# Performance work log

Measured on AMD Instinct MI355X. Metric: run time of the kernel, lower is better.

The kernel has to match this reference:

```python
import jax, jax.numpy as jnp
import numpy as np

N = 50000        # n_nodes
E = 640000       # n_edges
D = 128          # d_model (in_dim == out_dim)
H = 8            # num_heads
DH = D // H      # head dim = 16
EPS = 1e-5


def _batchnorm(x, g, b):
    # BatchNorm1d, training-mode batch statistics (biased variance)
    mu = jnp.mean(x, axis=0)
    var = jnp.mean((x - mu) ** 2, axis=0)
    return (x - mu) * jax.lax.rsqrt(var + EPS) * g + b


def setup_inputs() -> dict:
    key = jax.random.key(0)
    ks = jax.random.split(key, 16)
    s = 0.05
    h = jax.random.normal(ks[0], (N, D), jnp.float32)
    src = jax.random.randint(ks[1], (E,), 0, N)
    # guarantee every node has >= 1 incoming edge (avoids z == 0)
    dst = jnp.concatenate([jnp.arange(N), jax.random.randint(ks[2], (E - N,), 0, N)])
    return {
        "h": h,
        "src": src,
        "dst": dst,
        "WQ": jax.random.normal(ks[3], (D, D), jnp.float32) * s,
        "WK": jax.random.normal(ks[4], (D, D), jnp.float32) * s,
        "WV": jax.random.normal(ks[5], (D, D), jnp.float32) * s,
        "WO": jax.random.normal(ks[6], (D, D), jnp.float32) * s,
        "bO": jnp.zeros((D,), jnp.float32),
        "W1": jax.random.normal(ks[7], (2 * D, D), jnp.float32) * s,
        "b1": jnp.zeros((2 * D,), jnp.float32),
        "W2": jax.random.normal(ks[8], (D, 2 * D), jnp.float32) * s,
        "b2": jnp.zeros((D,), jnp.float32),
        "bn1_g": jnp.ones((D,), jnp.float32),
        "bn1_b": jnp.zeros((D,), jnp.float32),
        "bn2_g": jnp.ones((D,), jnp.float32),
        "bn2_b": jnp.zeros((D,), jnp.float32),
    }


def reference(h, src, dst, WQ, WK, WV, WO, bO, W1, b1, W2, b2, bn1_g, bn1_b, bn2_g, bn2_b):
    n = h.shape[0]
    # projections -> [N, H, DH]
    Q = (h @ WQ.T).reshape(n, H, DH)
    K = (h @ WK.T).reshape(n, H, DH)
    V = (h @ WV.T).reshape(n, H, DH)
    # per-edge score: sum(K[src] * Q[dst]) -> [E, H]; clamp/exp (scaled_exp)
    score = jnp.sum(K[src] * Q[dst], axis=-1) / np.sqrt(DH)
    score = jnp.exp(jnp.clip(score, -5.0, 5.0))
    # scatter-sum weighted values and normalizers to destination nodes
    wV = jax.ops.segment_sum(V[src] * score[..., None], dst, num_segments=n)  # [N,H,DH]
    z = jax.ops.segment_sum(score, dst, num_segments=n)                       # [N,H]
    attn = (wV / z[..., None]).reshape(n, D)
    # O projection + residual + BN1
    h1 = _batchnorm(h + (attn @ WO.T + bO), bn1_g, bn1_b)
    # FFN + residual + BN2
    f = jax.nn.relu(h1 @ W1.T + b1) @ W2.T + b2
    return _batchnorm(h1 + f, bn2_g, bn2_b)
```

## Files before the change

kernel.cpp:

```cpp
#include <hip/hip_runtime.h>
#include <math.h>


#define ND128 16384
typedef _Float16 f16;
typedef __attribute__((ext_vector_type(8))) _Float16 h8;
typedef __attribute__((ext_vector_type(4))) _Float16 h4;
typedef __attribute__((ext_vector_type(2))) _Float16 h2;
typedef __attribute__((ext_vector_type(4))) float f4;

__device__ __forceinline__ float fdot2h(h2 a, h2 b) {
#if __has_builtin(__builtin_amdgcn_fdot2)
    return __builtin_amdgcn_fdot2(a, b, 0.f, false);
#else
    return (float)a[0] * (float)b[0] + (float)a[1] * (float)b[1];
#endif
}

__device__ __forceinline__ float fast_exp2(float x) {
#if __has_builtin(__builtin_amdgcn_exp2f)
    return __builtin_amdgcn_exp2f(x);
#else
    return exp2f(x);
#endif
}

template <int CTRL>
__device__ __forceinline__ float dppadd(float x) {
    int t = __builtin_amdgcn_update_dpp(0, __float_as_int(x), CTRL, 0xF, 0xF, false);
    return x + __int_as_float(t);
}
__device__ __forceinline__ float wsum8(float p) {
    p = dppadd<0xB1>(p);
    p = dppadd<0x4E>(p);
    p = dppadd<0x141>(p);
    return p;
}

__global__ __launch_bounds__(256) void k_prep(
    const float* __restrict__ h, f16* __restrict__ hb,
    const float* __restrict__ WQ, const float* __restrict__ WK,
    const float* __restrict__ WV, const float* __restrict__ WO,
    const float* __restrict__ W2,
    f16* __restrict__ Wqb, f16* __restrict__ Wkb,
    f16* __restrict__ Wvb, f16* __restrict__ Wob, f16* __restrict__ W2b,
    float* __restrict__ bn, int* __restrict__ cursor, int N)
{
    const int slab = blockIdx.x, my = blockIdx.y;
    const int tid = threadIdx.x;
    if (my == 0) {
        if (tid < 128) {
            int ci = slab * 128 + tid;
            if (ci < N) cursor[ci] = 0;
        }
        if (slab == 6) { bn[tid] = 0.f; bn[tid + 256] = 0.f; }
    }
#pragma unroll
    for (int it2 = 0; it2 < 4; ++it2) {
        int it = my * 4 + it2;
        int cid = it * 256 + tid;
        int lane = cid & 63;
        int m = (cid >> 6) & 7;
        int kb = cid >> 9;
        int row = slab * 128 + m * 16 + (lane & 15);
        int col = kb * 32 + (lane >> 4) * 8;
        f16 o8[8];
        if (row < N) {
            const float* p = h + (size_t)row * 128 + col;
            float4 f0 = *(const float4*)p;
            float4 f1 = *(const float4*)(p + 4);
            o8[0] = (f16)f0.x; o8[1] = (f16)f0.y; o8[2] = (f16)f0.z; o8[3] = (f16)f0.w;
            o8[4] = (f16)f1.x; o8[5] = (f16)f1.y; o8[6] = (f16)f1.z; o8[7] = (f16)f1.w;
        } else {
#pragma unroll
            for (int j = 0; j < 8; ++j) o8[j] = (f16)0.f;
        }
        *(h8*)(hb + (size_t)slab * ND128 + (size_t)cid * 8) = *(const h8*)o8;
    }
    if (slab < 6 && my == 1) {
        const float* Wsrc; f16* dst; int K, base;
        if (slab < 4) {
            Wsrc = slab == 0 ? WQ : slab == 1 ? WK : slab == 2 ? WV : WO;
            dst  = slab == 0 ? Wqb : slab == 1 ? Wkb : slab == 2 ? Wvb : Wob;
            K = 128; base = 0;
        } else {
            Wsrc = W2; dst = W2b; K = 256; base = (slab - 4) * 2048;
        }
#pragma unroll
        for (int it = 0; it < 8; ++it) {
            int cid = base + it * 256 + tid;
            int lane = cid & 63;
            int kb, nt;
            if (K == 128) { kb = (cid >> 6) & 3; nt = cid >> 8; }
            else          { kb = (cid >> 6) & 7; nt = cid >> 9; }
            int row = nt * 16 + (lane & 15);
            int col = kb * 32 + (lane >> 4) * 8;
            const float* p = Wsrc + (size_t)row * K + col;
            f16 o8[8];
#pragma unroll
            for (int j = 0; j < 8; ++j) o8[j] = (f16)p[j];
            *(h8*)(dst + (size_t)cid * 8) = *(const h8*)o8;
        }
    }
}

__global__ __launch_bounds__(256) void k_qkv(
    const f16* __restrict__ hb, const f16* __restrict__ Wqb,
    const f16* __restrict__ Wkb, const f16* __restrict__ Wvb,
    f16* __restrict__ Qb, f16* __restrict__ Kh,
    f16* __restrict__ Vh, int N)
{
    const int slab = blockIdx.x, oidx = blockIdx.y, mh = blockIdx.z;
    const int w = threadIdx.x >> 6, lane = threadIdx.x & 63;
    const f16* __restrict__ Wb = oidx == 0 ? Wqb : oidx == 1 ? Wkb : Wvb;
    f16* __restrict__ Ob = oidx == 0 ? Qb : oidx == 1 ? Kh : Vh;
    const f16* A = hb + (size_t)slab * ND128;

    h8 bfr[2][4];
#pragma unroll
    for (int nt = 0; nt < 2; ++nt)
#pragma unroll
        for (int kb = 0; kb < 4; ++kb)
            bfr[nt][kb] = *(const h8*)(Wb + (size_t)(((2 * w + nt) * 4 + kb) * 64 + lane) * 8);

    f4 acc[4][2];
    f4 zero = {0.f, 0.f, 0.f, 0.f};
#pragma unroll
    for (int m = 0; m < 4; ++m) { acc[m][0] = zero; acc[m][1] = zero; }

#pragma unroll
    for (int m = 0; m < 4; ++m) {
        int mg = mh * 4 + m;
#pragma unroll
        for (int kb = 0; kb < 4; ++kb) {
            h8 a = *(const h8*)(A + (size_t)((kb * 8 + mg) * 64 + lane) * 8);
            acc[m][0] = __builtin_amdgcn_mfma_f32_16x16x32_f16(bfr[0][kb], a, acc[m][0], 0, 0, 0);
            acc[m][1] = __builtin_amdgcn_mfma_f32_16x16x32_f16(bfr[1][kb], a, acc[m][1], 0, 0, 0);
        }
    }

    const int rl = lane & 15, quad = lane >> 4;
#pragma unroll
    for (int m = 0; m < 4; ++m) {
        int gr = slab * 128 + (mh * 4 + m) * 16 + rl;
        if (gr < N) {
#pragma unroll
            for (int nt = 0; nt < 2; ++nt) {
                h4 o;
                o[0] = (f16)acc[m][nt][0]; o[1] = (f16)acc[m][nt][1];
                o[2] = (f16)acc[m][nt][2]; o[3] = (f16)acc[m][nt][3];
                *(h4*)(Ob + (size_t)gr * 128 + w * 32 + nt * 16 + quad * 4) = o;
            }
        }
    }
}

__global__ __launch_bounds__(256) void k_hist(
    const int* __restrict__ dst, int* __restrict__ cursor, int E)
{
    int e = blockIdx.x * 256 + threadIdx.x;
    if (e < E) atomicAdd(&cursor[dst[e]], 1);
}

__global__ __launch_bounds__(256) void k_scanA(
    const int* __restrict__ cnt, int* __restrict__ bsum, int N)
{
    const int t = threadIdx.x;
    int base = blockIdx.x * 2048 + t * 8;
    int s = 0;
#pragma unroll
    for (int j = 0; j < 8; ++j) {
        int idx = base + j;
        if (idx < N) s += cnt[idx];
    }
#pragma unroll
    for (int off = 32; off; off >>= 1) s += __shfl_down(s, off, 64);
    __shared__ int ws4[4];
    if ((t & 63) == 0) ws4[t >> 6] = s;
    __syncthreads();
    if (t == 0) bsum[blockIdx.x] = ws4[0] + ws4[1] + ws4[2] + ws4[3];
}

__global__ __launch_bounds__(256) void k_scanC(
    const int* __restrict__ cnt, const int* __restrict__ bsum,
    int* __restrict__ rowptr, int* __restrict__ cursor, int N, int nsb)
{
    const int t = threadIdx.x, b = blockIdx.x;
    __shared__ int sboff;
    if (t == 0) {
        int r = 0;
        for (int i2 = 0; i2 < b; ++i2) r += bsum[i2];
        sboff = r;
    }
    if (t == 64 && b == nsb - 1) {
        int r = 0;
        for (int i2 = 0; i2 < nsb; ++i2) r += bsum[i2];
        rowptr[N] = r;
    }
    int base = b * 2048 + t * 8;
    int loc[8];
    int s = 0;
#pragma unroll
    for (int j = 0; j < 8; ++j) {
        int idx = base + j;
        loc[j] = (idx < N) ? cnt[idx] : 0;
        s += loc[j];
    }
    __shared__ int part[256];
    part[t] = s;
    __syncthreads();
    for (int off = 1; off < 256; off <<= 1) {
        int v = (t >= off) ? part[t - off] : 0;
        __syncthreads();
        part[t] += v;
        __syncthreads();
    }
    int run = sboff + (t ? part[t - 1] : 0);
#pragma unroll
    for (int j = 0; j < 8; ++j) {
        int idx = base + j;
        if (idx < N) { rowptr[idx] = run; cursor[idx] = run; run += loc[j]; }
    }
}

__global__ __launch_bounds__(256) void k_scatter(
    const int* __restrict__ src, const int* __restrict__ dst,
    int* __restrict__ cursor, int* __restrict__ csr_src, int E)
{
    int e = blockIdx.x * 256 + threadIdx.x;
    if (e < E) {
        int pos = atomicAdd(&cursor[dst[e]], 1);
        csr_src[pos] = src[e];
    }
}

__global__ __launch_bounds__(256) void k_attn(
    const f16* __restrict__ Qb, const f16* __restrict__ Kh,
    const f16* __restrict__ Vh,
    const int* __restrict__ rowptr, const int* __restrict__ csr_src,
    f16* __restrict__ attnf, int N)
{
    const int node = blockIdx.x * 4 + (threadIdx.x >> 6);
    const int lane = threadIdx.x & 63;
    if (node >= N) return;
    const int beg = rowptr[node], end = rowptr[node + 1];

    h2 qs;
    {
        h2 q2 = ((const h2*)(Qb + (size_t)node * 128))[lane];
        const float SCL = 0.25f * 1.44269504f;
        qs[0] = (f16)((float)q2[0] * SCL);
        qs[1] = (f16)((float)q2[1] * SCL);
    }
    const float CLP = 5.f * 1.44269504f;

    const h2* __restrict__ K2 = (const h2*)Kh;
    const h2* __restrict__ V2 = (const h2*)Vh;

    h2 accA, accB;
    accA[0] = (f16)0.f; accA[1] = (f16)0.f;
    accB[0] = (f16)0.f; accB[1] = (f16)0.f;
    float z = 0.f;

    int i = beg;
    for (; i + 3 < end; i += 4) {
        int s0 = csr_src[i], s1 = csr_src[i + 1];
        int s2 = csr_src[i + 2], s3 = csr_src[i + 3];
        h2 k0 = K2[(size_t)s0 * 64 + lane];
        h2 k1 = K2[(size_t)s1 * 64 + lane];
        h2 k2 = K2[(size_t)s2 * 64 + lane];
        h2 k3 = K2[(size_t)s3 * 64 + lane];
        h2 v0 = V2[(size_t)s0 * 64 + lane];
        h2 v1 = V2[(size_t)s1 * 64 + lane];
        h2 v2 = V2[(size_t)s2 * 64 + lane];
        h2 v3 = V2[(size_t)s3 * 64 + lane];
        float p0 = fdot2h(qs, k0);
        float p1 = fdot2h(qs, k1);
        float p2 = fdot2h(qs, k2);
        float p3 = fdot2h(qs, k3);
        p0 = wsum8(p0); p1 = wsum8(p1); p2 = wsum8(p2); p3 = wsum8(p3);
        float sc0 = fast_exp2(fminf(fmaxf(p0, -CLP), CLP));
        float sc1 = fast_exp2(fminf(fmaxf(p1, -CLP), CLP));
        float sc2 = fast_exp2(fminf(fmaxf(p2, -CLP), CLP));
        float sc3 = fast_exp2(fminf(fmaxf(p3, -CLP), CLP));
        z += sc0 + sc1 + sc2 + sc3;
        h2 c0; c0[0] = (f16)sc0; c0[1] = (f16)sc0;
        h2 c1; c1[0] = (f16)sc1; c1[1] = (f16)sc1;
        h2 c2; c2[0] = (f16)sc2; c2[1] = (f16)sc2;
        h2 c3; c3[0] = (f16)sc3; c3[1] = (f16)sc3;
        accA += c0 * v0; accB += c1 * v1;
        accA += c2 * v2; accB += c3 * v3;
    }
    for (; i < end; ++i) {
        int s0 = csr_src[i];
        h2 k0 = K2[(size_t)s0 * 64 + lane];
        h2 v0 = V2[(size_t)s0 * 64 + lane];
        float p0 = fdot2h(qs, k0);
        p0 = wsum8(p0);
        float sc0 = fast_exp2(fminf(fmaxf(p0, -CLP), CLP));
        z += sc0;
        h2 c0; c0[0] = (f16)sc0; c0[1] = (f16)sc0;
        accA += c0 * v0;
    }

    float inv = 1.f / z;
    float ax = ((float)accA[0] + (float)accB[0]) * inv;
    float ay = ((float)accA[1] + (float)accB[1]) * inv;
    h2 o2;
    o2[0] = (f16)ax; o2[1] = (f16)ay;
    int slab = node >> 7, m = (node >> 4) & 7, lr = node & 15;
    int kb = lane >> 4, quad2 = (lane & 15) >> 2, j = (lane & 3) * 2;
    *(h2*)(attnf + (size_t)slab * ND128 +
           (size_t)(((kb * 8 + m) * 64 + lr + 16 * quad2) * 8 + j)) = o2;
}

__global__ __launch_bounds__(256) void k_oproj(
    const f16* __restrict__ attnf, const f16* __restrict__ Wob,
    const float* __restrict__ h, const float* __restrict__ bO,
    f16* __restrict__ t1b, float* __restrict__ bn, int N)
{
    __shared__ float csum[128], csq[128];
    const int tid = threadIdx.x, slab = blockIdx.x, mh = blockIdx.y;
    const int w = tid >> 6, lane = tid & 63;
    if (tid < 128) { csum[tid] = 0.f; csq[tid] = 0.f; }
    __syncthreads();
    const f16* A = attnf + (size_t)slab * ND128;

    h8 bfr[2][4];
#pragma unroll
    for (int nt = 0; nt < 2; ++nt)
#pragma unroll
        for (int kb = 0; kb < 4; ++kb)
            bfr[nt][kb] = *(const h8*)(Wob + (size_t)(((2 * w + nt) * 4 + kb) * 64 + lane) * 8);

    f4 acc[4][2];
    f4 zero = {0.f, 0.f, 0.f, 0.f};
#pragma unroll
    for (int m = 0; m < 4; ++m) { acc[m][0] = zero; acc[m][1] = zero; }
#pragma unroll
    for (int m = 0; m < 4; ++m) {
        int mg = mh * 4 + m;
#pragma unroll
        for (int kb = 0; kb < 4; ++kb) {
            h8 a = *(const h8*)(A + (size_t)((kb * 8 + mg) * 64 + lane) * 8);
            acc[m][0] = __builtin_amdgcn_mfma_f32_16x16x32_f16(bfr[0][kb], a, acc[m][0], 0, 0, 0);
            acc[m][1] = __builtin_amdgcn_mfma_f32_16x16x32_f16(bfr[1][kb], a, acc[m][1], 0, 0, 0);
        }
    }

    const int rl = lane & 15, quad = lane >> 4;
    float4 bo[2];
#pragma unroll
    for (int nt = 0; nt < 2; ++nt)
        bo[nt] = *(const float4*)(bO + w * 32 + nt * 16 + quad * 4);
    float pcs[2][4], pcq[2][4];
#pragma unroll
    for (int nt = 0; nt < 2; ++nt)
#pragma unroll
        for (int r = 0; r < 4; ++r) { pcs[nt][r] = 0.f; pcq[nt][r] = 0.f; }

#pragma unroll
    for (int m = 0; m < 4; ++m) {
        int mg = mh * 4 + m;
        int gr = slab * 128 + mg * 16 + rl;
        if (gr < N) {
#pragma unroll
            for (int nt = 0; nt < 2; ++nt) {
                int col0 = w * 32 + nt * 16 + quad * 4;
                float4 hv = *(const float4*)(h + (size_t)gr * 128 + col0);
                float v0 = acc[m][nt][0] + hv.x + bo[nt].x;
                float v1 = acc[m][nt][1] + hv.y + bo[nt].y;
                float v2 = acc[m][nt][2] + hv.z + bo[nt].z;
                float v3 = acc[m][nt][3] + hv.w + bo[nt].w;
                h4 o; o[0] = (f16)v0; o[1] = (f16)v1; o[2] = (f16)v2; o[3] = (f16)v3;
                *(h4*)(t1b + (size_t)slab * ND128 +
                       (size_t)(((w * 8 + mg) * 64 + (nt * 2 + (quad >> 1)) * 16 + rl) * 8 +
                                (quad & 1) * 4)) = o;
                pcs[nt][0] += v0; pcq[nt][0] += v0 * v0;
                pcs[nt][1] += v1; pcq[nt][1] += v1 * v1;
                pcs[nt][2] += v2; pcq[nt][2] += v2 * v2;
                pcs[nt][3] += v3; pcq[nt][3] += v3 * v3;
            }
        }
    }
#pragma unroll
    for (int nt = 0; nt < 2; ++nt)
#pragma unroll
        for (int r = 0; r < 4; ++r) {
            float s = pcs[nt][r], q = pcq[nt][r];
            s += __shfl_xor(s, 8, 16); q += __shfl_xor(q, 8, 16);
            s += __shfl_xor(s, 4, 16); q += __shfl_xor(q, 4, 16);
            s += __shfl_xor(s, 2, 16); q += __shfl_xor(q, 2, 16);
            s += __shfl_xor(s, 1, 16); q += __shfl_xor(q, 1, 16);
            if (rl == 0) {
                int cl = w * 32 + nt * 16 + quad * 4 + r;
                atomicAdd(&csum[cl], s);
                atomicAdd(&csq[cl], q);
            }
        }
    __syncthreads();
    if (tid < 128) {
        atomicAdd(bn + tid, csum[tid]);
        atomicAdd(bn + 128 + tid, csq[tid]);
    }
}

__global__ __launch_bounds__(128) void k_fold1(
    const float* __restrict__ bn, const float* __restrict__ g1,
    const float* __restrict__ bb1, const float* __restrict__ W1,
    const float* __restrict__ b1, f16* __restrict__ W1b,
    float* __restrict__ badj, float* __restrict__ sfold,
    float* __restrict__ bfold, int N)
{
    const int o = blockIdx.x, i = threadIdx.x;
    float invN = 1.f / (float)N;
    float mu = bn[i] * invN;
    float var = bn[128 + i] * invN - mu * mu;
    float s = g1[i] * rsqrtf(var + 1e-5f);
    float bb = bb1[i] - mu * s;
    if (o == 0) { sfold[i] = s; bfold[i] = bb; }
    float wv = W1[(size_t)o * 128 + i];
    __shared__ float red[128];
    red[i] = wv * bb;
    const int nt = o >> 4, lanelow = o & 15;
    const int kb = i >> 5, quad = (i >> 3) & 3, j = i & 7;
    W1b[(size_t)(((nt * 4 + kb) * 64 + lanelow + 16 * quad) * 8 + j)] = (f16)(wv * s);
    __syncthreads();
#pragma unroll
    for (int off = 64; off; off >>= 1) {
        if (i < off) red[i] += red[i + off];
        __syncthreads();
    }
    if (i == 0) badj[o] = b1[o] + red[0];
}

__global__ __launch_bounds__(256) void k_ffn1(
    const f16* __restrict__ t1b, const f16* __restrict__ W1b,
    const float* __restrict__ badj, f16* __restrict__ ub, int N)
{
    const int slab = blockIdx.x, ch = blockIdx.y, mh = blockIdx.z;
    const int w = threadIdx.x >> 6, lane = threadIdx.x & 63;
    const f16* A = t1b + (size_t)slab * ND128;

    h8 bfr[2][4];
#pragma unroll
    for (int nt = 0; nt < 2; ++nt)
#pragma unroll
        for (int kb = 0; kb < 4; ++kb) {
            int ntg = ch * 8 + 2 * w + nt;
            bfr[nt][kb] = *(const h8*)(W1b + (size_t)((ntg * 4 + kb) * 64 + lane) * 8);
        }

    f4 acc[4][2];
    f4 zero = {0.f, 0.f, 0.f, 0.f};
#pragma unroll
    for (int m = 0; m < 4; ++m) { acc[m][0] = zero; acc[m][1] = zero; }
#pragma unroll
    for (int m = 0; m < 4; ++m) {
        int mg = mh * 4 + m;
#pragma unroll
        for (int kb = 0; kb < 4; ++kb) {
            h8 a = *(const h8*)(A + (size_t)((kb * 8 + mg) * 64 + lane) * 8);
            acc[m][0] = __builtin_amdgcn_mfma_f32_16x16x32_f16(bfr[0][kb], a, acc[m][0], 0, 0, 0);
            acc[m][1] = __builtin_amdgcn_mfma_f32_16x16x32_f16(bfr[1][kb], a, acc[m][1], 0, 0, 0);
        }
    }

    const int rl = lane & 15, quad = lane >> 4;
    const int kbu = ch * 4 + w;
    float4 ba[2];
#pragma unroll
    for (int nt = 0; nt < 2; ++nt)
        ba[nt] = *(const float4*)(badj + ch * 128 + w * 32 + nt * 16 + quad * 4);
#pragma unroll
    for (int m = 0; m < 4; ++m) {
        int mg = mh * 4 + m;
        int gr = slab * 128 + mg * 16 + rl;
        if (gr < N) {
#pragma unroll
            for (int nt = 0; nt < 2; ++nt) {
                h4 o;
                o[0] = (f16)fmaxf(acc[m][nt][0] + ba[nt].x, 0.f);
                o[1] = (f16)fmaxf(acc[m][nt][1] + ba[nt].y, 0.f);
                o[2] = (f16)fmaxf(acc[m][nt][2] + ba[nt].z, 0.f);
                o[3] = (f16)fmaxf(acc[m][nt][3] + ba[nt].w, 0.f);
                *(h4*)(ub + (size_t)slab * 32768 +
                       (size_t)(((kbu * 8 + mg) * 64 + (nt * 2 + (quad >> 1)) * 16 + rl) * 8 +
                                (quad & 1) * 4)) = o;
            }
        }
    }
}

__global__ __launch_bounds__(256) void k_ffn2(
    const f16* __restrict__ ub, const f16* __restrict__ W2b,
    const f16* __restrict__ t1b,
    const float* __restrict__ sfold, const float* __restrict__ bfold,
    const float* __restrict__ b2, float* __restrict__ out,
    float* __restrict__ bn, int N)
{
    __shared__ float csum[128], csq[128], sS[128], sB[128];
    const int tid = threadIdx.x, slab = blockIdx.x, mh = blockIdx.y;
    const int w = tid >> 6, lane = tid & 63;
    if (tid < 128) {
        csum[tid] = 0.f; csq[tid] = 0.f;
        sS[tid] = sfold[tid]; sB[tid] = bfold[tid] + b2[tid];
    }
    __syncthreads();
    const f16* A = ub + (size_t)slab * 32768;
    const f16* T1 = t1b + (size_t)slab * ND128;

    h8 bfr[2][8];
#pragma unroll
    for (int nt = 0; nt < 2; ++nt)
#pragma unroll
        for (int kb = 0; kb < 8; ++kb)
            bfr[nt][kb] = *(const h8*)(W2b + (size_t)(((2 * w + nt) * 8 + kb) * 64 + lane) * 8);

    f4 acc[4][2];
    f4 zero = {0.f, 0.f, 0.f, 0.f};
#pragma unroll
    for (int m = 0; m < 4; ++m) { acc[m][0] = zero; acc[m][1] = zero; }
#pragma unroll
    for (int m = 0; m < 4; ++m) {
        int mg = mh * 4 + m;
#pragma unroll
        for (int kb = 0; kb < 8; ++kb) {
            h8 a = *(const h8*)(A + (size_t)((kb * 8 + mg) * 64 + lane) * 8);
            acc[m][0] = __builtin_amdgcn_mfma_f32_16x16x32_f16(bfr[0][kb], a, acc[m][0], 0, 0, 0);
            acc[m][1] = __builtin_amdgcn_mfma_f32_16x16x32_f16(bfr[1][kb], a, acc[m][1], 0, 0, 0);
        }
    }

    const int rl = lane & 15, quad = lane >> 4;
    float pcs[2][4], pcq[2][4];
#pragma unroll
    for (int nt = 0; nt < 2; ++nt)
#pragma unroll
        for (int r = 0; r < 4; ++r) { pcs[nt][r] = 0.f; pcq[nt][r] = 0.f; }

#pragma unroll
    for (int m = 0; m < 4; ++m) {
        int mg = mh * 4 + m;
        int gr = slab * 128 + mg * 16 + rl;
        if (gr < N) {
#pragma unroll
            for (int nt = 0; nt < 2; ++nt) {
                int col0 = w * 32 + nt * 16 + quad * 4;
                h4 t1v = *(const h4*)(T1 +
                    (size_t)(((w * 8 + mg) * 64 + (nt * 2 + (quad >> 1)) * 16 + rl) * 8 +
                             (quad & 1) * 4));
                float4 ss = *(const float4*)&sS[col0];
                float4 sb = *(const float4*)&sB[col0];
                float4 o;
                o.x = acc[m][nt][0] + fmaf(ss.x, (float)t1v[0], sb.x);
                o.y = acc[m][nt][1] + fmaf(ss.y, (float)t1v[1], sb.y);
                o.z = acc[m][nt][2] + fmaf(ss.z, (float)t1v[2], sb.z);
                o.w = acc[m][nt][3] + fmaf(ss.w, (float)t1v[3], sb.w);
                *(float4*)(out + (size_t)gr * 128 + col0) = o;
                pcs[nt][0] += o.x; pcq[nt][0] += o.x * o.x;
                pcs[nt][1] += o.y; pcq[nt][1] += o.y * o.y;
                pcs[nt][2] += o.z; pcq[nt][2] += o.z * o.z;
                pcs[nt][3] += o.w; pcq[nt][3] += o.w * o.w;
            }
        }
    }
#pragma unroll
    for (int nt = 0; nt < 2; ++nt)
#pragma unroll
        for (int r = 0; r < 4; ++r) {
            float s = pcs[nt][r], q = pcq[nt][r];
            s += __shfl_xor(s, 8, 16); q += __shfl_xor(q, 8, 16);
            s += __shfl_xor(s, 4, 16); q += __shfl_xor(q, 4, 16);
            s += __shfl_xor(s, 2, 16); q += __shfl_xor(q, 2, 16);
            s += __shfl_xor(s, 1, 16); q += __shfl_xor(q, 1, 16);
            if (rl == 0) {
                int cl = w * 32 + nt * 16 + quad * 4 + r;
                atomicAdd(&csum[cl], s);
                atomicAdd(&csq[cl], q);
            }
        }
    __syncthreads();
    if (tid < 128) {
        atomicAdd(bn + 256 + tid, csum[tid]);
        atomicAdd(bn + 384 + tid, csq[tid]);
    }
}

__global__ __launch_bounds__(256) void k_bn2(
    float* __restrict__ out, const float* __restrict__ bn,
    const float* __restrict__ g2, const float* __restrict__ bb2, int N)
{
    __shared__ float sS[128], sB[128];
    const int tid = threadIdx.x;
    if (tid < 128) {
        float invN = 1.f / (float)N;
        float mu = bn[256 + tid] * invN;
        float var = bn[384 + tid] * invN - mu * mu;
        float scl = g2[tid] * rsqrtf(var + 1e-5f);
        sS[tid] = scl;
        sB[tid] = bb2[tid] - mu * scl;
    }
    __syncthreads();
    size_t idx = (size_t)blockIdx.x * 256 + tid;
    size_t total = (size_t)N * 32;
    if (idx < total) {
        int c0 = (int)((idx * 4) & 127);
        float4 v = *(const float4*)(out + idx * 4);
        v.x = fmaf(v.x, sS[c0 + 0], sB[c0 + 0]);
        v.y = fmaf(v.y, sS[c0 + 1], sB[c0 + 1]);
        v.z = fmaf(v.z, sS[c0 + 2], sB[c0 + 2]);
        v.w = fmaf(v.w, sS[c0 + 3], sB[c0 + 3]);
        *(float4*)(out + idx * 4) = v;
    }
}

extern "C" void kernel_launch(void* const* d_in, const int* in_sizes, int n_in,
                              void* d_out, int out_size, void* d_ws, size_t ws_size,
                              hipStream_t stream)
{
    const float* h   = (const float*)d_in[0];
    const int*   src = (const int*)d_in[1];
    const int*   dst = (const int*)d_in[2];
    const float* WQ  = (const float*)d_in[3];
    const float* WK  = (const float*)d_in[4];
    const float* WV  = (const float*)d_in[5];
    const float* WO  = (const float*)d_in[6];
    const float* bO  = (const float*)d_in[7];
    const float* W1  = (const float*)d_in[8];
    const float* b1  = (const float*)d_in[9];
    const float* W2  = (const float*)d_in[10];
    const float* b2  = (const float*)d_in[11];
    const float* g1  = (const float*)d_in[12];
    const float* bb1 = (const float*)d_in[13];
    const float* g2  = (const float*)d_in[14];
    const float* bb2 = (const float*)d_in[15];
    float* out = (float*)d_out;

    int N = in_sizes[0] / 128;
    int E = in_sizes[1];
    const int slabs = (N + 127) / 128;
    const int nsb = (N + 2047) / 2048;
    const size_t B1 = (size_t)slabs * 32768;

    char* Wp = (char*)d_ws;
    f16* hb  = (f16*)Wp;
    f16* Qb  = (f16*)(Wp + B1);
    f16* Kh  = (f16*)(Wp + 2 * B1);
    f16* Vh  = (f16*)(Wp + 3 * B1);
    f16* ub  = (f16*)(Wp + B1);
    f16* t1b = (f16*)(Wp + 3 * B1);
    const size_t base = 4 * B1;
    f16* Wqb = (f16*)(Wp + base);
    f16* Wkb = (f16*)(Wp + base + 32768);
    f16* Wvb = (f16*)(Wp + base + 65536);
    f16* Wob = (f16*)(Wp + base + 98304);
    f16* W1b = (f16*)(Wp + base + 131072);
    f16* W2b = (f16*)(Wp + base + 196608);
    float* badj  = (float*)(Wp + base + 262144);
    float* sfold = (float*)(Wp + base + 263168);
    float* bfold = (float*)(Wp + base + 263680);
    float* bn    = (float*)(Wp + base + 264192);
    int* cursor  = (int*)(Wp + base + 266240);
    int* rowptr  = (int*)(Wp + base + 266240 + (size_t)N * 4);
    int* csr     = (int*)(Wp + base + 266240 + (size_t)N * 8 + 8);
    int* bsum    = (int*)((char*)csr + (size_t)E * 4);

    k_prep<<<dim3(slabs, 2), 256, 0, stream>>>(h, hb, WQ, WK, WV, WO, W2,
                                               Wqb, Wkb, Wvb, Wob, W2b, bn, cursor, N);
    k_qkv<<<dim3(slabs, 3, 2), 256, 0, stream>>>(hb, Wqb, Wkb, Wvb, Qb, Kh, Vh, N);
    k_hist<<<(E + 255) / 256, 256, 0, stream>>>(dst, cursor, E);
    k_scanA<<<nsb, 256, 0, stream>>>(cursor, bsum, N);
    k_scanC<<<nsb, 256, 0, stream>>>(cursor, bsum, rowptr, cursor, N, nsb);
    k_scatter<<<(E + 255) / 256, 256, 0, stream>>>(src, dst, cursor, csr, E);
    k_attn<<<(N + 3) / 4, 256, 0, stream>>>(Qb, Kh, Vh, rowptr, csr, hb, N);
    k_oproj<<<dim3(slabs, 2), 256, 0, stream>>>(hb, Wob, h, bO, t1b, bn, N);
    k_fold1<<<256, 128, 0, stream>>>(bn, g1, bb1, W1, b1, W1b, badj, sfold, bfold, N);
    k_ffn1<<<dim3(slabs, 2, 2), 256, 0, stream>>>(t1b, W1b, badj, ub, N);
    k_ffn2<<<dim3(slabs, 2), 256, 0, stream>>>(ub, W2b, t1b, sfold, bfold, b2, out, bn, N);
    k_bn2<<<(int)(((size_t)N * 32 + 255) / 256), 256, 0, stream>>>(out, bn, g2, bb2, N);
}
```

Baseline: 329.0 us.

## Store K/V in FP8, fuse hist into prep, merge tail kernels with grid barriers

K and V are now written by the QKV kernel as an interleaved FP8 buffer (256 bytes per node), halving the gather bytes in the edge-attention kernel, which decodes them to fp32 and accumulates in fp32. The degree histogram is merged into the prep kernel, and a memset replaces the in-kernel zeroing. The O-projection, BN1 fold, FFN1, FFN2 and BN2 kernels are collapsed into one persistent cooperative kernel that uses software grid barriers between phases, removing launch gaps. FP8 K/V lowers accuracy, and the spin barriers add synchronization cost and depend on every block being co-resident.

```diff
diff --git a/kernel.cpp b/kernel.cpp
--- a/kernel.cpp
+++ b/kernel.cpp
@@ -8,14 +8,7 @@
 typedef __attribute__((ext_vector_type(4))) _Float16 h4;
 typedef __attribute__((ext_vector_type(2))) _Float16 h2;
 typedef __attribute__((ext_vector_type(4))) float f4;
-
-__device__ __forceinline__ float fdot2h(h2 a, h2 b) {
-#if __has_builtin(__builtin_amdgcn_fdot2)
-    return __builtin_amdgcn_fdot2(a, b, 0.f, false);
-#else
-    return (float)a[0] * (float)b[0] + (float)a[1] * (float)b[1];
-#endif
-}
+typedef __attribute__((ext_vector_type(2))) float ff2;
 
 __device__ __forceinline__ float fast_exp2(float x) {
 #if __has_builtin(__builtin_amdgcn_exp2f)
@@ -37,24 +30,87 @@
     return p;
 }
 
-__global__ __launch_bounds__(256) void k_prep(
+__device__ __forceinline__ ff2 fp8x2_dec(unsigned v) {
+#if __has_builtin(__builtin_amdgcn_cvt_pk_f32_fp8)
+    return __builtin_amdgcn_cvt_pk_f32_fp8((int)v, false);
+#else
+    ff2 r;
+    unsigned b0 = v & 0xffu, b1 = (v >> 8) & 0xffu;
+    {
+        unsigned e = (b0 >> 3) & 15u, m = b0 & 7u;
+        float x = e ? __uint_as_float(((e + 120u) << 23) | (m << 20)) : (float)m * 0.001953125f;
+        r.x = (b0 & 0x80u) ? -x : x;
+    }
+    {
+        unsigned e = (b1 >> 3) & 15u, m = b1 & 7u;
+        float x = e ? __uint_as_float(((e + 120u) << 23) | (m << 20)) : (float)m * 0.001953125f;
+        r.y = (b1 & 0x80u) ? -x : x;
+    }
+    return r;
+#endif
+}
+
+#if !__has_builtin(__builtin_amdgcn_cvt_pk_fp8_f32)
+__device__ __forceinline__ unsigned char fp8_1(float f) {
+    float a = fabsf(f);
+    unsigned sg = (__float_as_uint(f) >> 31) << 7;
+    if (a >= 448.f) return (unsigned char)(sg | 0x7E);
+    if (a < 0.0009765625f) return (unsigned char)sg;
+    int E; float m = frexpf(a, &E);
+    if (E - 1 < -6) {
+        int q = (int)rintf(a * 512.f);
+        if (q > 7) return (unsigned char)(sg | 0x08);
+        return (unsigned char)(sg | q);
+    }
+    int q = (int)rintf(m * 16.f);
+    if (q == 16) { q = 8; E += 1; }
+    int Ef = E - 1 + 7;
+    if (Ef > 15) return (unsigned char)(sg | 0x7E);
+    return (unsigned char)(sg | (Ef << 3) | (q - 8));
+}
+#endif
+
+__device__ __forceinline__ unsigned fp8_pack4(float a0, float a1, float a2, float a3) {
+#if __has_builtin(__builtin_amdgcn_cvt_pk_fp8_f32)
+    int pk = __builtin_amdgcn_cvt_pk_fp8_f32(a0, a1, 0, false);
+    pk = __builtin_amdgcn_cvt_pk_fp8_f32(a2, a3, pk, true);
+    return (unsigned)pk;
+#else
+    return (unsigned)fp8_1(a0) | ((unsigned)fp8_1(a1) << 8) |
+           ((unsigned)fp8_1(a2) << 16) | ((unsigned)fp8_1(a3) << 24);
+#endif
+}
+
+__device__ __forceinline__ void gbar(int* cnt, int ph) {
+    __threadfence();
+    __syncthreads();
+    if (threadIdx.x == 0) {
+        __hip_atomic_fetch_add(cnt, 1, __ATOMIC_ACQ_REL, __HIP_MEMORY_SCOPE_AGENT);
+        const int target = (int)gridDim.x * ph;
+        while (__hip_atomic_load(cnt, __ATOMIC_ACQUIRE, __HIP_MEMORY_SCOPE_AGENT) < target)
+            __builtin_amdgcn_s_sleep(8);
+    }
+    __syncthreads();
+}
+
+__global__ __launch_bounds__(256) void k_prep_hist(
     const float* __restrict__ h, f16* __restrict__ hb,
     const float* __restrict__ WQ, const float* __restrict__ WK,
     const float* __restrict__ WV, const float* __restrict__ WO,
     const float* __restrict__ W2,
     f16* __restrict__ Wqb, f16* __restrict__ Wkb,
     f16* __restrict__ Wvb, f16* __restrict__ Wob, f16* __restrict__ W2b,
-    float* __restrict__ bn, int* __restrict__ cursor, int N)
+    int* __restrict__ cursor, const int* __restrict__ dst,
+    int N, int E, int nhb)
 {
-    const int slab = blockIdx.x, my = blockIdx.y;
     const int tid = threadIdx.x;
-    if (my == 0) {
-        if (tid < 128) {
-            int ci = slab * 128 + tid;
-            if (ci < N) cursor[ci] = 0;
-        }
-        if (slab == 6) { bn[tid] = 0.f; bn[tid + 256] = 0.f; }
-    }
+    if (blockIdx.x < (unsigned)nhb) {
+        int e = blockIdx.x * 256 + tid;
+        if (e < E) atomicAdd(&cursor[dst[e]], 1);
+        return;
+    }
+    const int p = blockIdx.x - nhb;
+    const int slab = p >> 1, my = p & 1;
 #pragma unroll
     for (int it2 = 0; it2 < 4; ++it2) {
         int it = my * 4 + it2;
@@ -66,9 +122,9 @@
         int col = kb * 32 + (lane >> 4) * 8;
         f16 o8[8];
         if (row < N) {
-            const float* p = h + (size_t)row * 128 + col;
-            float4 f0 = *(const float4*)p;
-            float4 f1 = *(const float4*)(p + 4);
+            const float* pp = h + (size_t)row * 128 + col;
+            float4 f0 = *(const float4*)pp;
+            float4 f1 = *(const float4*)(pp + 4);
             o8[0] = (f16)f0.x; o8[1] = (f16)f0.y; o8[2] = (f16)f0.z; o8[3] = (f16)f0.w;
             o8[4] = (f16)f1.x; o8[5] = (f16)f1.y; o8[6] = (f16)f1.z; o8[7] = (f16)f1.w;
         } else {
@@ -78,13 +134,13 @@
         *(h8*)(hb + (size_t)slab * ND128 + (size_t)cid * 8) = *(const h8*)o8;
     }
     if (slab < 6 && my == 1) {
-        const float* Wsrc; f16* dst; int K, base;
+        const float* Wsrc; f16* dstw; int K, base;
         if (slab < 4) {
             Wsrc = slab == 0 ? WQ : slab == 1 ? WK : slab == 2 ? WV : WO;
-            dst  = slab == 0 ? Wqb : slab == 1 ? Wkb : slab == 2 ? Wvb : Wob;
+            dstw = slab == 0 ? Wqb : slab == 1 ? Wkb : slab == 2 ? Wvb : Wob;
             K = 128; base = 0;
         } else {
-            Wsrc = W2; dst = W2b; K = 256; base = (slab - 4) * 2048;
+            Wsrc = W2; dstw = W2b; K = 256; base = (slab - 4) * 2048;
         }
 #pragma unroll
         for (int it = 0; it < 8; ++it) {
@@ -95,11 +151,11 @@
             else          { kb = (cid >> 6) & 7; nt = cid >> 9; }
             int row = nt * 16 + (lane & 15);
             int col = kb * 32 + (lane >> 4) * 8;
-            const float* p = Wsrc + (size_t)row * K + col;
+            const float* pp = Wsrc + (size_t)row * K + col;
             f16 o8[8];
 #pragma unroll
-            for (int j = 0; j < 8; ++j) o8[j] = (f16)p[j];
-            *(h8*)(dst + (size_t)cid * 8) = *(const h8*)o8;
+            for (int j = 0; j < 8; ++j) o8[j] = (f16)pp[j];
+            *(h8*)(dstw + (size_t)cid * 8) = *(const h8*)o8;
         }
     }
 }
@@ -107,13 +163,11 @@
 __global__ __launch_bounds__(256) void k_qkv(
     const f16* __restrict__ hb, const f16* __restrict__ Wqb,
     const f16* __restrict__ Wkb, const f16* __restrict__ Wvb,
-    f16* __restrict__ Qb, f16* __restrict__ Kh,
-    f16* __restrict__ Vh, int N)
+    f16* __restrict__ Qb, unsigned char* __restrict__ KV8, int N)
 {
     const int slab = blockIdx.x, oidx = blockIdx.y, mh = blockIdx.z;
     const int w = threadIdx.x >> 6, lane = threadIdx.x & 63;
     const f16* __restrict__ Wb = oidx == 0 ? Wqb : oidx == 1 ? Wkb : Wvb;
-    f16* __restrict__ Ob = oidx == 0 ? Qb : oidx == 1 ? Kh : Vh;
     const f16* A = hb + (size_t)slab * ND128;
 
     h8 bfr[2][4];
@@ -140,26 +194,35 @@
     }
 
     const int rl = lane & 15, quad = lane >> 4;
-#pragma unroll
-    for (int m = 0; m < 4; ++m) {
-        int gr = slab * 128 + (mh * 4 + m) * 16 + rl;
-        if (gr < N) {
-#pragma unroll
-            for (int nt = 0; nt < 2; ++nt) {
-                h4 o;
-                o[0] = (f16)acc[m][nt][0]; o[1] = (f16)acc[m][nt][1];
-                o[2] = (f16)acc[m][nt][2]; o[3] = (f16)acc[m][nt][3];
-                *(h4*)(Ob + (size_t)gr * 128 + w * 32 + nt * 16 + quad * 4) = o;
-            }
-        }
-    }
-}
-
-__global__ __launch_bounds__(256) void k_hist(
-    const int* __restrict__ dst, int* __restrict__ cursor, int E)
-{
-    int e = blockIdx.x * 256 + threadIdx.x;
-    if (e < E) atomicAdd(&cursor[dst[e]], 1);
+    if (oidx == 0) {
+#pragma unroll
+        for (int m = 0; m < 4; ++m) {
+            int gr = slab * 128 + (mh * 4 + m) * 16 + rl;
+            if (gr < N) {
+#pragma unroll
+                for (int nt = 0; nt < 2; ++nt) {
+                    h4 o;
+                    o[0] = (f16)acc[m][nt][0]; o[1] = (f16)acc[m][nt][1];
+                    o[2] = (f16)acc[m][nt][2]; o[3] = (f16)acc[m][nt][3];
+                    *(h4*)(Qb + (size_t)gr * 128 + w * 32 + nt * 16 + quad * 4) = o;
+                }
+            }
+        }
+    } else {
+        const int voff = (oidx == 2) ? 128 : 0;
+#pragma unroll
+        for (int m = 0; m < 4; ++m) {
+            int gr = slab * 128 + (mh * 4 + m) * 16 + rl;
+            if (gr < N) {
+#pragma unroll
+                for (int nt = 0; nt < 2; ++nt) {
+                    unsigned pk = fp8_pack4(acc[m][nt][0], acc[m][nt][1],
+                                            acc[m][nt][2], acc[m][nt][3]);
+                    *(unsigned*)(KV8 + (size_t)gr * 256 + voff + w * 32 + nt * 16 + quad * 4) = pk;
+                }
+            }
+        }
+    }
 }
 
 __global__ __launch_bounds__(256) void k_scanA(
@@ -235,8 +298,7 @@
 }
 
 __global__ __launch_bounds__(256) void k_attn(
-    const f16* __restrict__ Qb, const f16* __restrict__ Kh,
-    const f16* __restrict__ Vh,
+    const f16* __restrict__ Qb, const unsigned char* __restrict__ KV8,
     const int* __restrict__ rowptr, const int* __restrict__ csr_src,
     f16* __restrict__ attnf, int N)
 {
@@ -245,354 +307,341 @@
     if (node >= N) return;
     const int beg = rowptr[node], end = rowptr[node + 1];
 
-    h2 qs;
+    float qx, qy;
     {
         h2 q2 = ((const h2*)(Qb + (size_t)node * 128))[lane];
         const float SCL = 0.25f * 1.44269504f;
-        qs[0] = (f16)((float)q2[0] * SCL);
-        qs[1] = (f16)((float)q2[1] * SCL);
+        qx = (float)q2[0] * SCL;
+        qy = (float)q2[1] * SCL;
     }
     const float CLP = 5.f * 1.44269504f;
 
-    const h2* __restrict__ K2 = (const h2*)Kh;
-    const h2* __restrict__ V2 = (const h2*)Vh;
-
-    h2 accA, accB;
-    accA[0] = (f16)0.f; accA[1] = (f16)0.f;
-    accB[0] = (f16)0.f; accB[1] = (f16)0.f;
-    float z = 0.f;
-
+    float axA = 0.f, ayA = 0.f, axB = 0.f, ayB = 0.f, zA = 0.f, zB = 0.f;
     int i = beg;
     for (; i + 3 < end; i += 4) {
         int s0 = csr_src[i], s1 = csr_src[i + 1];
         int s2 = csr_src[i + 2], s3 = csr_src[i + 3];
-        h2 k0 = K2[(size_t)s0 * 64 + lane];
-        h2 k1 = K2[(size_t)s1 * 64 + lane];
-        h2 k2 = K2[(size_t)s2 * 64 + lane];
-        h2 k3 = K2[(size_t)s3 * 64 + lane];
-        h2 v0 = V2[(size_t)s0 * 64 + lane];
-        h2 v1 = V2[(size_t)s1 * 64 + lane];
-        h2 v2 = V2[(size_t)s2 * 64 + lane];
-        h2 v3 = V2[(size_t)s3 * 64 + lane];
-        float p0 = fdot2h(qs, k0);
-        float p1 = fdot2h(qs, k1);
-        float p2 = fdot2h(qs, k2);
-        float p3 = fdot2h(qs, k3);
+        unsigned k0 = *(const unsigned short*)(KV8 + (size_t)s0 * 256 + 2 * lane);
+        unsigned k1 = *(const unsigned short*)(KV8 + (size_t)s1 * 256 + 2 * lane);
+        unsigned k2 = *(const unsigned short*)(KV8 + (size_t)s2 * 256 + 2 * lane);
+        unsigned k3 = *(const unsigned short*)(KV8 + (size_t)s3 * 256 + 2 * lane);
+        unsigned v0 = *(const unsigned short*)(KV8 + (size_t)s0 * 256 + 128 + 2 * lane);
+        unsigned v1 = *(const unsigned short*)(KV8 + (size_t)s1 * 256 + 128 + 2 * lane);
+        unsigned v2 = *(const unsigned short*)(KV8 + (size_t)s2 * 256 + 128 + 2 * lane);
+        unsigned v3 = *(const unsigned short*)(KV8 + (size_t)s3 * 256 + 128 + 2 * lane);
+        ff2 kf0 = fp8x2_dec(k0), kf1 = fp8x2_dec(k1);
+        ff2 kf2 = fp8x2_dec(k2), kf3 = fp8x2_dec(k3);
+        float p0 = fmaf(qx, kf0.x, qy * kf0.y);
+        float p1 = fmaf(qx, kf1.x, qy * kf1.y);
+        float p2 = fmaf(qx, kf2.x, qy * kf2.y);
+        float p3 = fmaf(qx, kf3.x, qy * kf3.y);
         p0 = wsum8(p0); p1 = wsum8(p1); p2 = wsum8(p2); p3 = wsum8(p3);
         float sc0 = fast_exp2(fminf(fmaxf(p0, -CLP), CLP));
         float sc1 = fast_exp2(fminf(fmaxf(p1, -CLP), CLP));
         float sc2 = fast_exp2(fminf(fmaxf(p2, -CLP), CLP));
         float sc3 = fast_exp2(fminf(fmaxf(p3, -CLP), CLP));
-        z += sc0 + sc1 + sc2 + sc3;
-        h2 c0; c0[0] = (f16)sc0; c0[1] = (f16)sc0;
-        h2 c1; c1[0] = (f16)sc1; c1[1] = (f16)sc1;
-        h2 c2; c2[0] = (f16)sc2; c2[1] = (f16)sc2;
-        h2 c3; c3[0] = (f16)sc3; c3[1] = (f16)sc3;
-        accA += c0 * v0; accB += c1 * v1;
-        accA += c2 * v2; accB += c3 * v3;
+        ff2 vf0 = fp8x2_dec(v0), vf1 = fp8x2_dec(v1);
+        ff2 vf2 = fp8x2_dec(v2), vf3 = fp8x2_dec(v3);
+        axA = fmaf(vf0.x, sc0, axA); ayA = fmaf(vf0.y, sc0, ayA);
+        axB = fmaf(vf1.x, sc1, axB); ayB = fmaf(vf1.y, sc1, ayB);
+        axA = fmaf(vf2.x, sc2, axA); ayA = fmaf(vf2.y, sc2, ayA);
+        axB = fmaf(vf3.x, sc3, axB); ayB = fmaf(vf3.y, sc3, ayB);
+        zA += sc0 + sc2; zB += sc1 + sc3;
     }
     for (; i < end; ++i) {
         int s0 = csr_src[i];
-        h2 k0 = K2[(size_t)s0 * 64 + lane];
-        h2 v0 = V2[(size_t)s0 * 64 + lane];
-        float p0 = fdot2h(qs, k0);
+        unsigned k0 = *(const unsigned short*)(KV8 + (size_t)s0 * 256 + 2 * lane);
+        unsigned v0 = *(const unsigned short*)(KV8 + (size_t)s0 * 256 + 128 + 2 * lane);
+        ff2 kf0 = fp8x2_dec(k0);
+        float p0 = fmaf(qx, kf0.x, qy * kf0.y);
         p0 = wsum8(p0);
         float sc0 = fast_exp2(fminf(fmaxf(p0, -CLP), CLP));
-        z += sc0;
-        h2 c0; c0[0] = (f16)sc0; c0[1] = (f16)sc0;
-        accA += c0 * v0;
-    }
-
-    float inv = 1.f / z;
-    float ax = ((float)accA[0] + (float)accB[0]) * inv;
-    float ay = ((float)accA[1] + (float)accB[1]) * inv;
+        ff2 vf0 = fp8x2_dec(v0);
+        axA = fmaf(vf0.x, sc0, axA); ayA = fmaf(vf0.y, sc0, ayA);
+        zA += sc0;
+    }
+    float inv = 1.f / (zA + zB);
     h2 o2;
-    o2[0] = (f16)ax; o2[1] = (f16)ay;
+    o2[0] = (f16)((axA + axB) * inv);
+    o2[1] = (f16)((ayA + ayB) * inv);
     int slab = node >> 7, m = (node >> 4) & 7, lr = node & 15;
     int kb = lane >> 4, quad2 = (lane & 15) >> 2, j = (lane & 3) * 2;
     *(h2*)(attnf + (size_t)slab * ND128 +
            (size_t)(((kb * 8 + m) * 64 + lr + 16 * quad2) * 8 + j)) = o2;
 }
 
-__global__ __launch_bounds__(256) void k_oproj(
+__global__ __launch_bounds__(256) void k_backc(
     const f16* __restrict__ attnf, const f16* __restrict__ Wob,
     const float* __restrict__ h, const float* __restrict__ bO,
-    f16* __restrict__ t1b, float* __restrict__ bn, int N)
+    f16* __restrict__ t1b, float* __restrict__ bn,
+    const float* __restrict__ g1, const float* __restrict__ bb1,
+    const float* __restrict__ W1, const float* __restrict__ b1,
+    f16* __restrict__ W1b, float* __restrict__ badj,
+    float* __restrict__ sfold, float* __restrict__ bfold,
+    f16* __restrict__ ub, const f16* __restrict__ W2b,
+    const float* __restrict__ b2, float* __restrict__ out,
+    const float* __restrict__ g2, const float* __restrict__ bb2,
+    int* __restrict__ gcnt, int N, int slabs)
 {
-    __shared__ float csum[128], csq[128];
-    const int tid = threadIdx.x, slab = blockIdx.x, mh = blockIdx.y;
+    const int tid = threadIdx.x;
+    const int G = gridDim.x;
     const int w = tid >> 6, lane = tid & 63;
-    if (tid < 128) { csum[tid] = 0.f; csq[tid] = 0.f; }
-    __syncthreads();
-    const f16* A = attnf + (size_t)slab * ND128;
-
-    h8 bfr[2][4];
-#pragma unroll
-    for (int nt = 0; nt < 2; ++nt)
-#pragma unroll
-        for (int kb = 0; kb < 4; ++kb)
-            bfr[nt][kb] = *(const h8*)(Wob + (size_t)(((2 * w + nt) * 4 + kb) * 64 + lane) * 8);
-
-    f4 acc[4][2];
-    f4 zero = {0.f, 0.f, 0.f, 0.f};
-#pragma unroll
-    for (int m = 0; m < 4; ++m) { acc[m][0] = zero; acc[m][1] = zero; }
-#pragma unroll
-    for (int m = 0; m < 4; ++m) {
-        int mg = mh * 4 + m;
-#pragma unroll
-        for (int kb = 0; kb < 4; ++kb) {
-            h8 a = *(const h8*)(A + (size_t)((kb * 8 + mg) * 64 + lane) * 8);
-            acc[m][0] = __builtin_amdgcn_mfma_f32_16x16x32_f16(bfr[0][kb], a, acc[m][0], 0, 0, 0);
-            acc[m][1] = __builtin_amdgcn_mfma_f32_16x16x32_f16(bfr[1][kb], a, acc[m][1], 0, 0, 0);
-        }
-    }
-
     const int rl = lane & 15, quad = lane >> 4;
-    float4 bo[2];
-#pragma unroll
-    for (int nt = 0; nt < 2; ++nt)
-        bo[nt] = *(const float4*)(bO + w * 32 + nt * 16 + quad * 4);
-    float pcs[2][4], pcq[2][4];
-#pragma unroll
-    for (int nt = 0; nt < 2; ++nt)
-#pragma unroll
-        for (int r = 0; r < 4; ++r) { pcs[nt][r] = 0.f; pcq[nt][r] = 0.f; }
-
-#pragma unroll
-    for (int m = 0; m < 4; ++m) {
-        int mg = mh * 4 + m;
-        int gr = slab * 128 + mg * 16 + rl;
-        if (gr < N) {
-#pragma unroll
-            for (int nt = 0; nt < 2; ++nt) {
-                int col0 = w * 32 + nt * 16 + quad * 4;
-                float4 hv = *(const float4*)(h + (size_t)gr * 128 + col0);
-                float v0 = acc[m][nt][0] + hv.x + bo[nt].x;
-                float v1 = acc[m][nt][1] + hv.y + bo[nt].y;
-                float v2 = acc[m][nt][2] + hv.z + bo[nt].z;
-                float v3 = acc[m][nt][3] + hv.w + bo[nt].w;
-                h4 o; o[0] = (f16)v0; o[1] = (f16)v1; o[2] = (f16)v2; o[3] = (f16)v3;
-                *(h4*)(t1b + (size_t)slab * ND128 +
-                       (size_t)(((w * 8 + mg) * 64 + (nt * 2 + (quad >> 1)) * 16 + rl) * 8 +
-                                (quad & 1) * 4)) = o;
-                pcs[nt][0] += v0; pcq[nt][0] += v0 * v0;
-                pcs[nt][1] += v1; pcq[nt][1] += v1 * v1;
-                pcs[nt][2] += v2; pcq[nt][2] += v2 * v2;
-                pcs[nt][3] += v3; pcq[nt][3] += v3 * v3;
-            }
-        }
-    }
-#pragma unroll
-    for (int nt = 0; nt < 2; ++nt)
-#pragma unroll
-        for (int r = 0; r < 4; ++r) {
-            float s = pcs[nt][r], q = pcq[nt][r];
-            s += __shfl_xor(s, 8, 16); q += __shfl_xor(q, 8, 16);
-            s += __shfl_xor(s, 4, 16); q += __shfl_xor(q, 4, 16);
-            s += __shfl_xor(s, 2, 16); q += __shfl_xor(q, 2, 16);
-            s += __shfl_xor(s, 1, 16); q += __shfl_xor(q, 1, 16);
-            if (rl == 0) {
-                int cl = w * 32 + nt * 16 + quad * 4 + r;
-                atomicAdd(&csum[cl], s);
-                atomicAdd(&csq[cl], q);
-            }
-        }
-    __syncthreads();
-    if (tid < 128) {
-        atomicAdd(bn + tid, csum[tid]);
-        atomicAdd(bn + 128 + tid, csq[tid]);
-    }
-}
-
-__global__ __launch_bounds__(128) void k_fold1(
-    const float* __restrict__ bn, const float* __restrict__ g1,
-    const float* __restrict__ bb1, const float* __restrict__ W1,
-    const float* __restrict__ b1, f16* __restrict__ W1b,
-    float* __restrict__ badj, float* __restrict__ sfold,
-    float* __restrict__ bfold, int N)
-{
-    const int o = blockIdx.x, i = threadIdx.x;
-    float invN = 1.f / (float)N;
-    float mu = bn[i] * invN;
-    float var = bn[128 + i] * invN - mu * mu;
-    float s = g1[i] * rsqrtf(var + 1e-5f);
-    float bb = bb1[i] - mu * s;
-    if (o == 0) { sfold[i] = s; bfold[i] = bb; }
-    float wv = W1[(size_t)o * 128 + i];
+    __shared__ float csum[128], csq[128], sS[128], sB[128];
     __shared__ float red[128];
-    red[i] = wv * bb;
-    const int nt = o >> 4, lanelow = o & 15;
-    const int kb = i >> 5, quad = (i >> 3) & 3, j = i & 7;
-    W1b[(size_t)(((nt * 4 + kb) * 64 + lanelow + 16 * quad) * 8 + j)] = (f16)(wv * s);
-    __syncthreads();
-#pragma unroll
-    for (int off = 64; off; off >>= 1) {
-        if (i < off) red[i] += red[i + off];
+
+    {
+        h8 bfr[2][4];
+#pragma unroll
+        for (int nt = 0; nt < 2; ++nt)
+#pragma unroll
+            for (int kb = 0; kb < 4; ++kb)
+                bfr[nt][kb] = *(const h8*)(Wob + (size_t)(((2 * w + nt) * 4 + kb) * 64 + lane) * 8);
+        float4 bo[2];
+#pragma unroll
+        for (int nt = 0; nt < 2; ++nt)
+            bo[nt] = *(const float4*)(bO + w * 32 + nt * 16 + quad * 4);
+
+        for (int u = blockIdx.x; u < slabs * 2; u += G) {
+            const int slab = u >> 1, mh = u & 1;
+            if (tid < 128) { csum[tid] = 0.f; csq[tid] = 0.f; }
+            __syncthreads();
+            const f16* A = attnf + (size_t)slab * ND128;
+
+            f4 acc[4][2];
+            f4 zero = {0.f, 0.f, 0.f, 0.f};
+#pragma unroll
+            for (int m = 0; m < 4; ++m) { acc[m][0] = zero; acc[m][1] = zero; }
+#pragma unroll
+            for (int m = 0; m < 4; ++m) {
+                int mg = mh * 4 + m;
+#pragma unroll
+                for (int kb = 0; kb < 4; ++kb) {
+                    h8 a = *(const h8*)(A + (size_t)((kb * 8 + mg) * 64 + lane) * 8);
+                    acc[m][0] = __builtin_amdgcn_mfma_f32_16x16x32_f16(bfr[0][kb], a, acc[m][0], 0, 0, 0);
+                    acc[m][1] = __builtin_amdgcn_mfma_f32_16x16x32_f16(bfr[1][kb], a, acc[m][1], 0, 0, 0);
+                }
+            }
+            float pcs[2][4], pcq[2][4];
+#pragma unroll
+            for (int nt = 0; nt < 2; ++nt)
+#pragma unroll
+                for (int r = 0; r < 4; ++r) { pcs[nt][r] = 0.f; pcq[nt][r] = 0.f; }
+#pragma unroll
+            for (int m = 0; m < 4; ++m) {
+                int mg = mh * 4 + m;
+                int gr = slab * 128 + mg * 16 + rl;
+                if (gr < N) {
+#pragma unroll
+                    for (int nt = 0; nt < 2; ++nt) {
+                        int col0 = w * 32 + nt * 16 + quad * 4;
+                        float4 hv = *(const float4*)(h + (size_t)gr * 128 + col0);
+                        float v0 = acc[m][nt][0] + hv.x + bo[nt].x;
+                        float v1 = acc[m][nt][1] + hv.y + bo[nt].y;
+                        float v2 = acc[m][nt][2] + hv.z + bo[nt].z;
+                        float v3 = acc[m][nt][3] + hv.w + bo[nt].w;
+                        h4 o; o[0] = (f16)v0; o[1] = (f16)v1; o[2] = (f16)v2; o[3] = (f16)v3;
+                        *(h4*)(t1b + (size_t)slab * ND128 +
+                               (size_t)(((w * 8 + mg) * 64 + (nt * 2 + (quad >> 1)) * 16 + rl) * 8 +
+                                        (quad & 1) * 4)) = o;
+                        pcs[nt][0] += v0; pcq[nt][0] += v0 * v0;
+                        pcs[nt][1] += v1; pcq[nt][1] += v1 * v1;
+                        pcs[nt][2] += v2; pcq[nt][2] += v2 * v2;
+                        pcs[nt][3] += v3; pcq[nt][3] += v3 * v3;
+                    }
+                }
+            }
+#pragma unroll
+            for (int nt = 0; nt < 2; ++nt)
+#pragma unroll
+                for (int r = 0; r < 4; ++r) {
+                    float s = pcs[nt][r], q = pcq[nt][r];
+                    s += __shfl_xor(s, 8, 16); q += __shfl_xor(q, 8, 16);
+                    s += __shfl_xor(s, 4, 16); q += __shfl_xor(q, 4, 16);
+                    s += __shfl_xor(s, 2, 16); q += __shfl_xor(q, 2, 16);
+                    s += __shfl_xor(s, 1, 16); q += __shfl_xor(q, 1, 16);
+                    if (rl == 0) {
+                        int cl = w * 32 + nt * 16 + quad * 4 + r;
+                        atomicAdd(&csum[cl], s);
+                        atomicAdd(&csq[cl], q);
+                    }
+                }
+            __syncthreads();
+            if (tid < 128) {
+                atomicAdd(bn + tid, csum[tid]);
+                atomicAdd(bn + 128 + tid, csq[tid]);
+            }
+            __syncthreads();
+        }
+    }
+    gbar(gcnt, 1);
+
+    for (int u = blockIdx.x; u < 256; u += G) {
+        const int o = u;
+        if (tid < 128) {
+            const int i = tid;
+            float invN = 1.f / (float)N;
+            float mu = bn[i] * invN;
+            float var = bn[128 + i] * invN - mu * mu;
+            float s = g1[i] * rsqrtf(var + 1e-5f);
+            float bb = bb1[i] - mu * s;
+            if (o == 0) { sfold[i] = s; bfold[i] = bb; }
+            float wv = W1[(size_t)o * 128 + i];
+            red[i] = wv * bb;
+            const int nt = o >> 4, lanelow = o & 15;
+            const int kb = i >> 5, qq = (i >> 3) & 3, j = i & 7;
+            W1b[(size_t)(((nt * 4 + kb) * 64 + lanelow + 16 * qq) * 8 + j)] = (f16)(wv * s);
+        }
         __syncthreads();
-    }
-    if (i == 0) badj[o] = b1[o] + red[0];
-}
-
-__global__ __launch_bounds__(256) void k_ffn1(
-    const f16* __restrict__ t1b, const f16* __restrict__ W1b,
-    const float* __restrict__ badj, f16* __restrict__ ub, int N)
-{
-    const int slab = blockIdx.x, ch = blockIdx.y, mh = blockIdx.z;
-    const int w = threadIdx.x >> 6, lane = threadIdx.x & 63;
-    const f16* A = t1b + (size_t)slab * ND128;
-
-    h8 bfr[2][4];
-#pragma unroll
-    for (int nt = 0; nt < 2; ++nt)
-#pragma unroll
-        for (int kb = 0; kb < 4; ++kb) {
-            int ntg = ch * 8 + 2 * w + nt;
-            bfr[nt][kb] = *(const h8*)(W1b + (size_t)((ntg * 4 + kb) * 64 + lane) * 8);
-        }
-
-    f4 acc[4][2];
-    f4 zero = {0.f, 0.f, 0.f, 0.f};
-#pragma unroll
-    for (int m = 0; m < 4; ++m) { acc[m][0] = zero; acc[m][1] = zero; }
-#pragma unroll
-    for (int m = 0; m < 4; ++m) {
-        int mg = mh * 4 + m;
-#pragma unroll
-        for (int kb = 0; kb < 4; ++kb) {
-            h8 a = *(const h8*)(A + (size_t)((kb * 8 + mg) * 64 + lane) * 8);
-            acc[m][0] = __builtin_amdgcn_mfma_f32_16x16x32_f16(bfr[0][kb], a, acc[m][0], 0, 0, 0);
-            acc[m][1] = __builtin_amdgcn_mfma_f32_16x16x32_f16(bfr[1][kb], a, acc[m][1], 0, 0, 0);
-        }
-    }
-
-    const int rl = lane & 15, quad = lane >> 4;
-    const int kbu = ch * 4 + w;
-    float4 ba[2];
-#pragma unroll
-    for (int nt = 0; nt < 2; ++nt)
-        ba[nt] = *(const float4*)(badj + ch * 128 + w * 32 + nt * 16 + quad * 4);
-#pragma unroll
-    for (int m = 0; m < 4; ++m) {
-        int mg = mh * 4 + m;
-        int gr = slab * 128 + mg * 16 + rl;
-        if (gr < N) {
-#pragma unroll
-            for (int nt = 0; nt < 2; ++nt) {
-                h4 o;
-                o[0] = (f16)fmaxf(acc[m][nt][0] + ba[nt].x, 0.f);
-                o[1] = (f16)fmaxf(acc[m][nt][1] + ba[nt].y, 0.f);
-                o[2] = (f16)fmaxf(acc[m][nt][2] + ba[nt].z, 0.f);
-                o[3] = (f16)fmaxf(acc[m][nt][3] + ba[nt].w, 0.f);
-                *(h4*)(ub + (size_t)slab * 32768 +
-                       (size_t)(((kbu * 8 + mg) * 64 + (nt * 2 + (quad >> 1)) * 16 + rl) * 8 +
-                                (quad & 1) * 4)) = o;
-            }
-        }
-    }
-}
-
-__global__ __launch_bounds__(256) void k_ffn2(
-    const f16* __restrict__ ub, const f16* __restrict__ W2b,
-    const f16* __restrict__ t1b,
-    const float* __restrict__ sfold, const float* __restrict__ bfold,
-    const float* __restrict__ b2, float* __restrict__ out,
-    float* __restrict__ bn, int N)
-{
-    __shared__ float csum[128], csq[128], sS[128], sB[128];
-    const int tid = threadIdx.x, slab = blockIdx.x, mh = blockIdx.y;
-    const int w = tid >> 6, lane = tid & 63;
-    if (tid < 128) {
-        csum[tid] = 0.f; csq[tid] = 0.f;
-        sS[tid] = sfold[tid]; sB[tid] = bfold[tid] + b2[tid];
-    }
-    __syncthreads();
-    const f16* A = ub + (size_t)slab * 32768;
-    const f16* T1 = t1b + (size_t)slab * ND128;
-
-    h8 bfr[2][8];
-#pragma unroll
-    for (int nt = 0; nt < 2; ++nt)
-#pragma unroll
-        for (int kb = 0; kb < 8; ++kb)
-            bfr[nt][kb] = *(const h8*)(W2b + (size_t)(((2 * w + nt) * 8 + kb) * 64 + lane) * 8);
-
-    f4 acc[4][2];
-    f4 zero = {0.f, 0.f, 0.f, 0.f};
-#pragma unroll
-    for (int m = 0; m < 4; ++m) { acc[m][0] = zero; acc[m][1] = zero; }
-#pragma unroll
-    for (int m = 0; m < 4; ++m) {
-        int mg = mh * 4 + m;
-#pragma unroll
-        for (int kb = 0; kb < 8; ++kb) {
-            h8 a = *(const h8*)(A + (size_t)((kb * 8 + mg) * 64 + lane) * 8);
-            acc[m][0] = __builtin_amdgcn_mfma_f32_16x16x32_f16(bfr[0][kb], a, acc[m][0], 0, 0, 0);
-            acc[m][1] = __builtin_amdgcn_mfma_f32_16x16x32_f16(bfr[1][kb], a, acc[m][1], 0, 0, 0);
-        }
-    }
-
-    const int rl = lane & 15, quad = lane >> 4;
-    float pcs[2][4], pcq[2][4];
-#pragma unroll
-    for (int nt = 0; nt < 2; ++nt)
-#pragma unroll
-        for (int r = 0; r < 4; ++r) { pcs[nt][r] = 0.f; pcq[nt][r] = 0.f; }
-
-#pragma unroll
-    for (int m = 0; m < 4; ++m) {
-        int mg = mh * 4 + m;
-        int gr = slab * 128 + mg * 16 + rl;
-        if (gr < N) {
-#pragma unroll
-            for (int nt = 0; nt < 2; ++nt) {
-                int col0 = w * 32 + nt * 16 + quad * 4;
-                h4 t1v = *(const h4*)(T1 +
-                    (size_t)(((w * 8 + mg) * 64 + (nt * 2 + (quad >> 1)) * 16 + rl) * 8 +
-                             (quad & 1) * 4));
-                float4 ss = *(const float4*)&sS[col0];
-                float4 sb = *(const float4*)&sB[col0];
-                float4 o;
-                o.x = acc[m][nt][0] + fmaf(ss.x, (float)t1v[0], sb.x);
-                o.y = acc[m][nt][1] + fmaf(ss.y, (float)t1v[1], sb.y);
-                o.z = acc[m][nt][2] + fmaf(ss.z, (float)t1v[2], sb.z);
-                o.w = acc[m][nt][3] + fmaf(ss.w, (float)t1v[3], sb.w);
-                *(float4*)(out + (size_t)gr * 128 + col0) = o;
-                pcs[nt][0] += o.x; pcq[nt][0] += o.x * o.x;
-                pcs[nt][1] += o.y; pcq[nt][1] += o.y * o.y;
-                pcs[nt][2] += o.z; pcq[nt][2] += o.z * o.z;
-                pcs[nt][3] += o.w; pcq[nt][3] += o.w * o.w;
-            }
-        }
-    }
-#pragma unroll
-    for (int nt = 0; nt < 2; ++nt)
-#pragma unroll
-        for (int r = 0; r < 4; ++r) {
-            float s = pcs[nt][r], q = pcq[nt][r];
-            s += __shfl_xor(s, 8, 16); q += __shfl_xor(q, 8, 16);
-            s += __shfl_xor(s, 4, 16); q += __shfl_xor(q, 4, 16);
-            s += __shfl_xor(s, 2, 16); q += __shfl_xor(q, 2, 16);
-            s += __shfl_xor(s, 1, 16); q += __shfl_xor(q, 1, 16);
-            if (rl == 0) {
-                int cl = w * 32 + nt * 16 + quad * 4 + r;
-                atomicAdd(&csum[cl], s);
-                atomicAdd(&csq[cl], q);
-            }
-        }
-    __syncthreads();
-    if (tid < 128) {
-        atomicAdd(bn + 256 + tid, csum[tid]);
-        atomicAdd(bn + 384 + tid, csq[tid]);
-    }
-}
-
-__global__ __launch_bounds__(256) void k_bn2(
-    float* __restrict__ out, const float* __restrict__ bn,
-    const float* __restrict__ g2, const float* __restrict__ bb2, int N)
-{
-    __shared__ float sS[128], sB[128];
-    const int tid = threadIdx.x;
+        for (int off = 64; off; off >>= 1) {
+            if (tid < off) red[tid] += red[tid + off];
+            __syncthreads();
+        }
+        if (tid == 0) badj[o] = b1[o] + red[0];
+        __syncthreads();
+    }
+    gbar(gcnt, 2);
+
+    for (int u = blockIdx.x; u < slabs * 4; u += G) {
+        const int slab = u >> 2, ch = (u >> 1) & 1, mh = u & 1;
+        const f16* A = t1b + (size_t)slab * ND128;
+
+        h8 bfr[2][4];
+#pragma unroll
+        for (int nt = 0; nt < 2; ++nt)
+#pragma unroll
+            for (int kb = 0; kb < 4; ++kb) {
+                int ntg = ch * 8 + 2 * w + nt;
+                bfr[nt][kb] = *(const h8*)(W1b + (size_t)((ntg * 4 + kb) * 64 + lane) * 8);
+            }
+
+        f4 acc[4][2];
+        f4 zero = {0.f, 0.f, 0.f, 0.f};
+#pragma unroll
+        for (int m = 0; m < 4; ++m) { acc[m][0] = zero; acc[m][1] = zero; }
+#pragma unroll
+        for (int m = 0; m < 4; ++m) {
+            int mg = mh * 4 + m;
+#pragma unroll
+            for (int kb = 0; kb < 4; ++kb) {
+                h8 a = *(const h8*)(A + (size_t)((kb * 8 + mg) * 64 + lane) * 8);
+                acc[m][0] = __builtin_amdgcn_mfma_f32_16x16x32_f16(bfr[0][kb], a, acc[m][0], 0, 0, 0);
+                acc[m][1] = __builtin_amdgcn_mfma_f32_16x16x32_f16(bfr[1][kb], a, acc[m][1], 0, 0, 0);
+            }
+        }
+        const int kbu = ch * 4 + w;
+        float4 ba[2];
+#pragma unroll
+        for (int nt = 0; nt < 2; ++nt)
+            ba[nt] = *(const float4*)(badj + ch * 128 + w * 32 + nt * 16 + quad * 4);
+#pragma unroll
+        for (int m = 0; m < 4; ++m) {
+            int mg = mh * 4 + m;
+            int gr = slab * 128 + mg * 16 + rl;
+            if (gr < N) {
+#pragma unroll
+                for (int nt = 0; nt < 2; ++nt) {
+                    h4 o;
+                    o[0] = (f16)fmaxf(acc[m][nt][0] + ba[nt].x, 0.f);
+                    o[1] = (f16)fmaxf(acc[m][nt][1] + ba[nt].y, 0.f);
+                    o[2] = (f16)fmaxf(acc[m][nt][2] + ba[nt].z, 0.f);
+                    o[3] = (f16)fmaxf(acc[m][nt][3] + ba[nt].w, 0.f);
+                    *(h4*)(ub + (size_t)slab * 32768 +
+                           (size_t)(((kbu * 8 + mg) * 64 + (nt * 2 + (quad >> 1)) * 16 + rl) * 8 +
+                                    (quad & 1) * 4)) = o;
+                }
+            }
+        }
+    }
+    gbar(gcnt, 3);
+
+    {
+        h8 bfr[2][8];
+#pragma unroll
+        for (int nt = 0; nt < 2; ++nt)
+#pragma unroll
+            for (int kb = 0; kb < 8; ++kb)
+                bfr[nt][kb] = *(const h8*)(W2b + (size_t)(((2 * w + nt) * 8 + kb) * 64 + lane) * 8);
+        if (tid < 128) { sS[tid] = sfold[tid]; sB[tid] = bfold[tid] + b2[tid]; }
+        __syncthreads();
+
+        for (int u = blockIdx.x; u < slabs * 2; u += G) {
+            const int slab = u >> 1, mh = u & 1;
+            if (tid < 128) { csum[tid] = 0.f; csq[tid] = 0.f; }
+            __syncthreads();
+            const f16* A = ub + (size_t)slab * 32768;
+            const f16* T1 = t1b + (size_t)slab * ND128;
+
+            f4 acc[4][2];
+            f4 zero = {0.f, 0.f, 0.f, 0.f};
+#pragma unroll
+            for (int m = 0; m < 4; ++m) { acc[m][0] = zero; acc[m][1] = zero; }
+#pragma unroll
+            for (int m = 0; m < 4; ++m) {
+                int mg = mh * 4 + m;
+#pragma unroll
+                for (int kb = 0; kb < 8; ++kb) {
+                    h8 a = *(const h8*)(A + (size_t)((kb * 8 + mg) * 64 + lane) * 8);
+                    acc[m][0] = __builtin_amdgcn_mfma_f32_16x16x32_f16(bfr[0][kb], a, acc[m][0], 0, 0, 0);
+                    acc[m][1] = __builtin_amdgcn_mfma_f32_16x16x32_f16(bfr[1][kb], a, acc[m][1], 0, 0, 0);
+                }
+            }
+            float pcs[2][4], pcq[2][4];
+#pragma unroll
+            for (int nt = 0; nt < 2; ++nt)
+#pragma unroll
+                for (int r = 0; r < 4; ++r) { pcs[nt][r] = 0.f; pcq[nt][r] = 0.f; }
+#pragma unroll
+            for (int m = 0; m < 4; ++m) {
+                int mg = mh * 4 + m;
+                int gr = slab * 128 + mg * 16 + rl;
+                if (gr < N) {
+#pragma unroll
+                    for (int nt = 0; nt < 2; ++nt) {
+                        int col0 = w * 32 + nt * 16 + quad * 4;
+                        h4 t1v = *(const h4*)(T1 +
+                            (size_t)(((w * 8 + mg) * 64 + (nt * 2 + (quad >> 1)) * 16 + rl) * 8 +
+                                     (quad & 1) * 4));
+                        float4 ss = *(const float4*)&sS[col0];
+                        float4 sb = *(const float4*)&sB[col0];
+                        float4 o;
+                        o.x = acc[m][nt][0] + fmaf(ss.x, (float)t1v[0], sb.x);
+                        o.y = acc[m][nt][1] + fmaf(ss.y, (float)t1v[1], sb.y);
+                        o.z = acc[m][nt][2] + fmaf(ss.z, (float)t1v[2], sb.z);
+                        o.w = acc[m][nt][3] + fmaf(ss.w, (float)t1v[3], sb.w);
+                        *(float4*)(out + (size_t)gr * 128 + col0) = o;
+                        pcs[nt][0] += o.x; pcq[nt][0] += o.x * o.x;
+                        pcs[nt][1] += o.y; pcq[nt][1] += o.y * o.y;
+                        pcs[nt][2] += o.z; pcq[nt][2] += o.z * o.z;
+                        pcs[nt][3] += o.w; pcq[nt][3] += o.w * o.w;
+                    }
+                }
+            }
+#pragma unroll
+            for (int nt = 0; nt < 2; ++nt)
+#pragma unroll
+                for (int r = 0; r < 4; ++r) {
+                    float s = pcs[nt][r], q = pcq[nt][r];
+                    s += __shfl_xor(s, 8, 16); q += __shfl_xor(q, 8, 16);
+                    s += __shfl_xor(s, 4, 16); q += __shfl_xor(q, 4, 16);
+                    s += __shfl_xor(s, 2, 16); q += __shfl_xor(q, 2, 16);
+                    s += __shfl_xor(s, 1, 16); q += __shfl_xor(q, 1, 16);
+                    if (rl == 0) {
+                        int cl = w * 32 + nt * 16 + quad * 4 + r;
+                        atomicAdd(&csum[cl], s);
+                        atomicAdd(&csq[cl], q);
+                    }
+                }
+            __syncthreads();
+            if (tid < 128) {
+                atomicAdd(bn + 256 + tid, csum[tid]);
+                atomicAdd(bn + 384 + tid, csq[tid]);
+            }
+            __syncthreads();
+        }
+    }
+    gbar(gcnt, 4);
+
     if (tid < 128) {
         float invN = 1.f / (float)N;
         float mu = bn[256 + tid] * invN;
@@ -602,16 +651,19 @@
         sB[tid] = bb2[tid] - mu * scl;
     }
     __syncthreads();
-    size_t idx = (size_t)blockIdx.x * 256 + tid;
-    size_t total = (size_t)N * 32;
-    if (idx < total) {
-        int c0 = (int)((idx * 4) & 127);
-        float4 v = *(const float4*)(out + idx * 4);
-        v.x = fmaf(v.x, sS[c0 + 0], sB[c0 + 0]);
-        v.y = fmaf(v.y, sS[c0 + 1], sB[c0 + 1]);
-        v.z = fmaf(v.z, sS[c0 + 2], sB[c0 + 2]);
-        v.w = fmaf(v.w, sS[c0 + 3], sB[c0 + 3]);
-        *(float4*)(out + idx * 4) = v;
+    const size_t total = (size_t)N * 32;
+    const int U9 = (int)((total + 255) / 256);
+    for (int u = blockIdx.x; u < U9; u += G) {
+        size_t idx = (size_t)u * 256 + tid;
+        if (idx < total) {
+            int c0 = (int)((idx * 4) & 127);
+            float4 v = *(const float4*)(out + idx * 4);
+            v.x = fmaf(v.x, sS[c0 + 0], sB[c0 + 0]);
+            v.y = fmaf(v.y, sS[c0 + 1], sB[c0 + 1]);
+            v.z = fmaf(v.z, sS[c0 + 2], sB[c0 + 2]);
+            v.w = fmaf(v.w, sS[c0 + 3], sB[c0 + 3]);
+            *(float4*)(out + idx * 4) = v;
+        }
     }
 }
 
@@ -639,15 +691,15 @@
 
     int N = in_sizes[0] / 128;
     int E = in_sizes[1];
-    const int slabs = (N + 127) / 128;
-    const int nsb = (N + 2047) / 2048;
+    int slabs = (N + 127) / 128;
+    int nsb = (N + 2047) / 2048;
+    int nhb = (E + 255) / 256;
     const size_t B1 = (size_t)slabs * 32768;
 
     char* Wp = (char*)d_ws;
     f16* hb  = (f16*)Wp;
     f16* Qb  = (f16*)(Wp + B1);
-    f16* Kh  = (f16*)(Wp + 2 * B1);
-    f16* Vh  = (f16*)(Wp + 3 * B1);
+    unsigned char* KV8 = (unsigned char*)(Wp + 2 * B1);
     f16* ub  = (f16*)(Wp + B1);
     f16* t1b = (f16*)(Wp + 3 * B1);
     const size_t base = 4 * B1;
@@ -661,22 +713,38 @@
     float* sfold = (float*)(Wp + base + 263168);
     float* bfold = (float*)(Wp + base + 263680);
     float* bn    = (float*)(Wp + base + 264192);
-    int* cursor  = (int*)(Wp + base + 266240);
-    int* rowptr  = (int*)(Wp + base + 266240 + (size_t)N * 4);
-    int* csr     = (int*)(Wp + base + 266240 + (size_t)N * 8 + 8);
-    int* bsum    = (int*)((char*)csr + (size_t)E * 4);
-
-    k_prep<<<dim3(slabs, 2), 256, 0, stream>>>(h, hb, WQ, WK, WV, WO, W2,
-                                               Wqb, Wkb, Wvb, Wob, W2b, bn, cursor, N);
-    k_qkv<<<dim3(slabs, 3, 2), 256, 0, stream>>>(hb, Wqb, Wkb, Wvb, Qb, Kh, Vh, N);
-    k_hist<<<(E + 255) / 256, 256, 0, stream>>>(dst, cursor, E);
+    int* gcnt    = (int*)(Wp + base + 266240);
+    int* bsum    = (int*)(Wp + base + 266496);
+    int* cursor  = (int*)(Wp + base + 266752);
+    int* rowptr  = (int*)(Wp + base + 266752 + (size_t)N * 4);
+    int* csr     = (int*)(Wp + base + 266752 + (size_t)N * 8 + 8);
+
+    static int ncu = 0, nbk = 0;
+    if (ncu == 0) {
+        int dev = 0;
+        hipGetDevice(&dev);
+        hipDeviceGetAttribute(&ncu, hipDeviceAttributeMultiprocessorCount, dev);
+        hipOccupancyMaxActiveBlocksPerMultiprocessor(&nbk, k_backc, 256, 0);
+        if (ncu <= 0) ncu = 256;
+        if (nbk <= 0) nbk = 1;
+    }
+    int G2 = ncu * nbk;
+    if (G2 > slabs * 4) G2 = slabs * 4;
+
+    hipMemsetAsync(Wp + base + 264192, 0, 2560 + (size_t)N * 4, stream);
+    k_prep_hist<<<nhb + slabs * 2, 256, 0, stream>>>(
+        h, hb, WQ, WK, WV, WO, W2, Wqb, Wkb, Wvb, Wob, W2b, cursor, dst, N, E, nhb);
+    k_qkv<<<dim3(slabs, 3, 2), 256, 0, stream>>>(hb, Wqb, Wkb, Wvb, Qb, KV8, N);
     k_scanA<<<nsb, 256, 0, stream>>>(cursor, bsum, N);
     k_scanC<<<nsb, 256, 0, stream>>>(cursor, bsum, rowptr, cursor, N, nsb);
-    k_scatter<<<(E + 255) / 256, 256, 0, stream>>>(src, dst, cursor, csr, E);
-    k_attn<<<(N + 3) / 4, 256, 0, stream>>>(Qb, Kh, Vh, rowptr, csr, hb, N);
-    k_oproj<<<dim3(slabs, 2), 256, 0, stream>>>(hb, Wob, h, bO, t1b, bn, N);
-    k_fold1<<<256, 128, 0, stream>>>(bn, g1, bb1, W1, b1, W1b, badj, sfold, bfold, N);
-    k_ffn1<<<dim3(slabs, 2, 2), 256, 0, stream>>>(t1b, W1b, badj, ub, N);
-    k_ffn2<<<dim3(slabs, 2), 256, 0, stream>>>(ub, W2b, t1b, sfold, bfold, b2, out, bn, N);
-    k_bn2<<<(int)(((size_t)N * 32 + 255) / 256), 256, 0, stream>>>(out, bn, g2, bb2, N);
-}
+    k_scatter<<<nhb, 256, 0, stream>>>(src, dst, cursor, csr, E);
+    k_attn<<<(N + 3) / 4, 256, 0, stream>>>(Qb, KV8, rowptr, csr, hb, N);
+    {
+        void* a2[] = {(void*)&hb, (void*)&Wob, (void*)&h, (void*)&bO, (void*)&t1b,
+                      (void*)&bn, (void*)&g1, (void*)&bb1, (void*)&W1, (void*)&b1,
+                      (void*)&W1b, (void*)&badj, (void*)&sfold, (void*)&bfold,
+                      (void*)&ub, (void*)&W2b, (void*)&b2, (void*)&out,
+                      (void*)&g2, (void*)&bb2, (void*)&gcnt, (void*)&N, (void*)&slabs};
+        hipLaunchCooperativeKernel((void*)k_backc, dim3(G2), dim3(256), a2, 0, stream);
+    }
+}
```

After: 561.1 us. 1.71x slower.
